# Kernel tuning notes

Hardware: AMD Instinct MI355X
Metric: run time of the kernel (lower is better)

## Reference

```python
import jax, jax.numpy as jnp
import numpy as np

GAMMA = 0.1
EPS = 1e-10


def setup_inputs() -> dict:
    key = jax.random.key(0)
    ks = jax.random.split(key, 7)
    B, N, D = 1024, 2048, 128
    return {
        "target_embed": jax.random.normal(ks[0], (B, D), dtype=jnp.float32),
        "candidate_embeds": jax.random.normal(ks[1], (B, N, D), dtype=jnp.float32),
        "Wq": jax.random.normal(ks[2], (D, D), dtype=jnp.float32) * 0.05,
        "bq": jax.random.normal(ks[3], (D,), dtype=jnp.float32) * 0.05,
        "Wk": jax.random.normal(ks[4], (D, D), dtype=jnp.float32) * 0.05,
        "bk": jax.random.normal(ks[5], (D,), dtype=jnp.float32) * 0.05,
        "u": jax.random.uniform(ks[6], (B, N), dtype=jnp.float32),
        "num_neighbors": 32,
    }


def reference(target_embed, candidate_embeds, Wq, bq, Wk, bk, u, num_neighbors):
    B, N, D = candidate_embeds.shape
    scale = jnp.sqrt(jnp.float32(D))
    # Linear projections (torch Linear: x @ W.T + b)
    Q = target_embed @ Wq.T + bq                      # [B, D]
    K = jnp.einsum('bnd,ed->bne', candidate_embeds, Wk) + bk  # [B, N, D]
    scores = jnp.einsum('bd,bnd->bn', Q, K) / scale   # [B, N]
    p = jax.nn.softmax(scores, axis=-1)
    p = (1.0 - GAMMA) * p + GAMMA / N                 # mix with uniform
    # multinomial without replacement == Gumbel top-k on log-probs
    gumbel = -jnp.log(-jnp.log(u + EPS) + EPS)        # [B, N]
    _, sampled_idx = jax.lax.top_k(jnp.log(p) + gumbel, num_neighbors)  # [B, k]
    return sampled_idx
```

## Files before the change

### kernel.cpp

```cpp
#include <hip/hip_runtime.h>
#include <cmath>
#include <cfloat>

constexpr int D  = 128;
constexpr int NT = 512;
constexpr int NW = NT / 64;
constexpr float EPS_ = 1e-10f;

__global__ __launch_bounds__(NT, 8) void adaptive_sampler_kernel(
    const float* __restrict__ target,
    const float* __restrict__ cand,
    const float* __restrict__ Wq,
    const float* __restrict__ bq,
    const float* __restrict__ Wk,
    const float* __restrict__ u,
    const int*   __restrict__ kptr,
    int*         __restrict__ out,
    int N)
{
  extern __shared__ float sS[];
  __shared__ float sTgt[D];
  __shared__ float sQ[D];
  __shared__ float sQt[D];
  __shared__ float redV[NW];
  __shared__ int   redI[NW];

  const int b    = blockIdx.x;
  const int tid  = threadIdx.x;
  const int lane = tid & 63;
  const int wave = tid >> 6;

  if (tid < D) sTgt[tid] = target[(size_t)b * D + tid];
  __syncthreads();

  if (tid < D) {
    float acc = 0.f;
    const float* wrow = Wq + (size_t)tid * D;
    #pragma unroll 8
    for (int e = 0; e < D; ++e) acc += sTgt[e] * wrow[e];
    sQ[tid] = acc + bq[tid];
  }
  __syncthreads();

  if (tid < D) {
    float acc = 0.f;
    #pragma unroll 8
    for (int d = 0; d < D; ++d) acc += sQ[d] * Wk[(size_t)d * D + tid];
    sQt[tid] = acc;
  }
  __syncthreads();

  const int grp = lane >> 4;
  const int gl  = lane & 15;
  float q0 = sQt[gl * 8 + 0], q1 = sQt[gl * 8 + 1];
  float q2 = sQt[gl * 8 + 2], q3 = sQt[gl * 8 + 3];
  float q4 = sQt[gl * 8 + 4], q5 = sQt[gl * 8 + 5];
  float q6 = sQt[gl * 8 + 6], q7 = sQt[gl * 8 + 7];

  const float scale = sqrtf((float)D);
  const int rstride = NW * 4;

  int n = wave * 4 + grp;
  for (; n + rstride < N; n += 2 * rstride) {
    const float4* r0 = (const float4*)(cand + ((size_t)b * N + n) * D);
    const float4* r1 = (const float4*)(cand + ((size_t)b * N + n + rstride) * D);
    float4 a0 = r0[gl * 2 + 0];
    float4 a1 = r0[gl * 2 + 1];
    float4 c0 = r1[gl * 2 + 0];
    float4 c1 = r1[gl * 2 + 1];
    float p0 = a0.x * q0 + a0.y * q1 + a0.z * q2 + a0.w * q3
             + a1.x * q4 + a1.y * q5 + a1.z * q6 + a1.w * q7;
    float p1 = c0.x * q0 + c0.y * q1 + c0.z * q2 + c0.w * q3
             + c1.x * q4 + c1.y * q5 + c1.z * q6 + c1.w * q7;
    p0 += __shfl_xor(p0, 1);  p1 += __shfl_xor(p1, 1);
    p0 += __shfl_xor(p0, 2);  p1 += __shfl_xor(p1, 2);
    p0 += __shfl_xor(p0, 4);  p1 += __shfl_xor(p1, 4);
    p0 += __shfl_xor(p0, 8);  p1 += __shfl_xor(p1, 8);
    if (gl == 0) { sS[n] = p0 / scale; sS[n + rstride] = p1 / scale; }
  }
  if (n < N) {
    const float4* r0 = (const float4*)(cand + ((size_t)b * N + n) * D);
    float4 a0 = r0[gl * 2 + 0];
    float4 a1 = r0[gl * 2 + 1];
    float p0 = a0.x * q0 + a0.y * q1 + a0.z * q2 + a0.w * q3
             + a1.x * q4 + a1.y * q5 + a1.z * q6 + a1.w * q7;
    p0 += __shfl_xor(p0, 1);
    p0 += __shfl_xor(p0, 2);
    p0 += __shfl_xor(p0, 4);
    p0 += __shfl_xor(p0, 8);
    if (gl == 0) sS[n] = p0 / scale;
  }
  __syncthreads();

  float m = -FLT_MAX;
  for (int i = tid; i < N; i += NT) m = fmaxf(m, sS[i]);
  for (int s = 32; s; s >>= 1) m = fmaxf(m, __shfl_xor(m, s));
  if (lane == 0) redV[wave] = m;
  __syncthreads();
  m = redV[0];
  #pragma unroll
  for (int w = 1; w < NW; ++w) m = fmaxf(m, redV[w]);
  __syncthreads();

  float ssum = 0.f;
  for (int i = tid; i < N; i += NT) ssum += expf(sS[i] - m);
  for (int s = 32; s; s >>= 1) ssum += __shfl_xor(ssum, s);
  if (lane == 0) redV[wave] = ssum;
  __syncthreads();
  float Z = redV[0];
  #pragma unroll
  for (int w = 1; w < NW; ++w) Z += redV[w];
  __syncthreads();

  const float mixc = (float)(0.1 / (double)N);
  for (int i = tid; i < N; i += NT) {
    float pmix = 0.9f * (expf(sS[i] - m) / Z) + mixc;
    float uv = u[(size_t)b * N + i];
    float g = -logf(-logf(uv + EPS_) + EPS_);
    sS[i] = logf(pmix) + g;
  }
  __syncthreads();

  const int k = kptr[0];
  for (int i = 0; i < k; ++i) {
    float bv = -FLT_MAX;
    int   bi = N;
    for (int j = tid; j < N; j += NT) {
      float v = sS[j];
      if (v > bv || (v == bv && j < bi)) { bv = v; bi = j; }
    }
    for (int s = 32; s; s >>= 1) {
      float ov = __shfl_xor(bv, s);
      int   oi = __shfl_xor(bi, s);
      if (ov > bv || (ov == bv && oi < bi)) { bv = ov; bi = oi; }
    }
    if (lane == 0) { redV[wave] = bv; redI[wave] = bi; }
    __syncthreads();
    if (tid == 0) {
      float fv = redV[0]; int fi = redI[0];
      #pragma unroll
      for (int w = 1; w < NW; ++w) {
        if (redV[w] > fv || (redV[w] == fv && redI[w] < fi)) {
          fv = redV[w]; fi = redI[w];
        }
      }
      out[(size_t)b * k + i] = fi;
      sS[fi] = -FLT_MAX;
    }
    __syncthreads();
  }
}

extern "C" void kernel_launch(void* const* d_in, const int* in_sizes, int n_in,
                              void* d_out, int out_size, void* d_ws, size_t ws_size,
                              hipStream_t stream) {
  const float* target = (const float*)d_in[0];
  const float* cand   = (const float*)d_in[1];
  const float* Wq     = (const float*)d_in[2];
  const float* bq     = (const float*)d_in[3];
  const float* Wk     = (const float*)d_in[4];
  const float* bk     = (const float*)d_in[5];
  const float* u      = (const float*)d_in[6];
  const int*   kptr   = (const int*)d_in[7];
  (void)bk;
  (void)n_in; (void)d_ws; (void)ws_size; (void)out_size;

  const int B = in_sizes[0] / D;
  const int N = in_sizes[1] / (B * D);

  adaptive_sampler_kernel<<<B, NT, N * sizeof(float), stream>>>(
      target, cand, Wq, bq, Wk, u, kptr, (int*)d_out, N);
}
```

Before: 256.6 us.

## Split sampler into projection, chunked score, and register-resident top-k kernels

Splits the fused kernel into three kernels when workspace allows. A projection kernel computes the query vector, a score kernel spreads each batch row's 2048 candidates over four blocks to raise parallelism on the bandwidth-bound dot products, and a top-k kernel keeps scores in registers, does a per-wave top-k and merges candidates in one wave. This replaces k block-wide barriers with wave-level work. The cost is extra launches and a workspace round-trip for the scores. It falls back to the fused kernel if workspace is too small, and the default path depends on ws_size.

```diff
diff --git a/kernel.cpp b/kernel.cpp
--- a/kernel.cpp
+++ b/kernel.cpp
@@ -1,38 +1,193 @@
 #include <hip/hip_runtime.h>
 #include <cmath>
 #include <cfloat>
-
-constexpr int D  = 128;
-constexpr int NT = 512;
-constexpr int NW = NT / 64;
+#include <climits>
+
+constexpr int D    = 128;
 constexpr float EPS_ = 1e-10f;
-
-__global__ __launch_bounds__(NT, 8) void adaptive_sampler_kernel(
-    const float* __restrict__ target,
-    const float* __restrict__ cand,
-    const float* __restrict__ Wq,
-    const float* __restrict__ bq,
-    const float* __restrict__ Wk,
-    const float* __restrict__ u,
-    const int*   __restrict__ kptr,
-    int*         __restrict__ out,
-    int N)
+constexpr int KMAX = 64;
+
+__global__ __launch_bounds__(128) void proj_kernel(
+    const float* __restrict__ target, const float* __restrict__ Wq,
+    const float* __restrict__ bq, const float* __restrict__ Wk,
+    float* __restrict__ qt)
+{
+  __shared__ float sTgt[D];
+  __shared__ float sQ[D];
+  const int b = blockIdx.x, tid = threadIdx.x;
+  sTgt[tid] = target[(size_t)b * D + tid];
+  __syncthreads();
+  float acc = 0.f;
+  const float* wrow = Wq + (size_t)tid * D;
+  #pragma unroll 8
+  for (int e = 0; e < D; ++e) acc += sTgt[e] * wrow[e];
+  sQ[tid] = acc + bq[tid];
+  __syncthreads();
+  acc = 0.f;
+  #pragma unroll 8
+  for (int d = 0; d < D; ++d) acc += sQ[d] * Wk[(size_t)d * D + tid];
+  qt[(size_t)b * D + tid] = acc;
+}
+
+constexpr int NT1 = 256;
+__global__ __launch_bounds__(NT1, 8) void score_kernel(
+    const float* __restrict__ cand, const float* __restrict__ qt,
+    float* __restrict__ scores, int N, int rows_per_blk)
+{
+  const int b    = blockIdx.x;
+  const int tid  = threadIdx.x;
+  const int lane = tid & 63;
+  const int wave = tid >> 6;
+  const int grp  = lane >> 4;
+  const int gl   = lane & 15;
+
+  const float* qp = qt + (size_t)b * D + gl * 8;
+  float4 qa = ((const float4*)qp)[0];
+  float4 qb = ((const float4*)qp)[1];
+
+  const float scale = sqrtf((float)D);
+  const int n0 = blockIdx.y * rows_per_blk;
+  const int n1 = n0 + rows_per_blk;
+  const float* base = cand + (size_t)b * N * D;
+  float* srow = scores + (size_t)b * N;
+
+  for (int n = n0 + wave * 4 + grp; n < n1; n += 32) {
+    const float4* r0 = (const float4*)(base + (size_t)n * D);
+    const float4* r1 = (const float4*)(base + (size_t)(n + 16) * D);
+    float4 a0 = r0[gl * 2 + 0];
+    float4 a1 = r0[gl * 2 + 1];
+    float4 c0 = r1[gl * 2 + 0];
+    float4 c1 = r1[gl * 2 + 1];
+    float p0 = a0.x * qa.x + a0.y * qa.y + a0.z * qa.z + a0.w * qa.w
+             + a1.x * qb.x + a1.y * qb.y + a1.z * qb.z + a1.w * qb.w;
+    float p1 = c0.x * qa.x + c0.y * qa.y + c0.z * qa.z + c0.w * qa.w
+             + c1.x * qb.x + c1.y * qb.y + c1.z * qb.z + c1.w * qb.w;
+    p0 += __shfl_xor(p0, 1);  p1 += __shfl_xor(p1, 1);
+    p0 += __shfl_xor(p0, 2);  p1 += __shfl_xor(p1, 2);
+    p0 += __shfl_xor(p0, 4);  p1 += __shfl_xor(p1, 4);
+    p0 += __shfl_xor(p0, 8);  p1 += __shfl_xor(p1, 8);
+    if (gl == 0) { srow[n] = p0 / scale; srow[n + 16] = p1 / scale; }
+  }
+}
+
+constexpr int NT2 = 256;
+__global__ __launch_bounds__(NT2) void topk_kernel(
+    const float* __restrict__ scores, const float* __restrict__ u,
+    const int* __restrict__ kptr, int* __restrict__ out, int N)
+{
+  __shared__ float redM[4];
+  __shared__ float redS[4];
+  __shared__ float cV[4 * KMAX];
+  __shared__ int   cI[4 * KMAX];
+
+  const int b    = blockIdx.x;
+  const int tid  = threadIdx.x;
+  const int lane = tid & 63;
+  const int wave = tid >> 6;
+  const int base = wave * 512 + lane * 8;
+
+  const float* srow = scores + (size_t)b * N;
+  float4 s0 = ((const float4*)(srow + base))[0];
+  float4 s1 = ((const float4*)(srow + base))[1];
+  float v[8] = { s0.x, s0.y, s0.z, s0.w, s1.x, s1.y, s1.z, s1.w };
+
+  float m = v[0];
+  #pragma unroll
+  for (int j = 1; j < 8; ++j) m = fmaxf(m, v[j]);
+  for (int s = 32; s; s >>= 1) m = fmaxf(m, __shfl_xor(m, s));
+  if (lane == 0) redM[wave] = m;
+  __syncthreads();
+  m = fmaxf(fmaxf(redM[0], redM[1]), fmaxf(redM[2], redM[3]));
+
+  float ssum = 0.f;
+  #pragma unroll
+  for (int j = 0; j < 8; ++j) ssum += expf(v[j] - m);
+  for (int s = 32; s; s >>= 1) ssum += __shfl_xor(ssum, s);
+  if (lane == 0) redS[wave] = ssum;
+  __syncthreads();
+  const float Z = redS[0] + redS[1] + redS[2] + redS[3];
+
+  const float mixc = (float)(0.1 / (double)N);
+  const float* urow = u + (size_t)b * N;
+  float4 u0 = ((const float4*)(urow + base))[0];
+  float4 u1 = ((const float4*)(urow + base))[1];
+  float uu[8] = { u0.x, u0.y, u0.z, u0.w, u1.x, u1.y, u1.z, u1.w };
+  #pragma unroll
+  for (int j = 0; j < 8; ++j) {
+    float pmix = 0.9f * (expf(v[j] - m) / Z) + mixc;
+    float g = -logf(-logf(uu[j] + EPS_) + EPS_);
+    v[j] = logf(pmix) + g;
+  }
+
+  const int k = kptr[0];
+
+  for (int i = 0; i < k; ++i) {
+    float bv = v[0]; int bj = 0;
+    #pragma unroll
+    for (int j = 1; j < 8; ++j) if (v[j] > bv) { bv = v[j]; bj = j; }
+    int bidx = base + bj;
+    for (int s = 32; s; s >>= 1) {
+      float ov = __shfl_xor(bv, s);
+      int   oi = __shfl_xor(bidx, s);
+      if (ov > bv || (ov == bv && oi < bidx)) { bv = ov; bidx = oi; }
+    }
+    if (lane == ((bidx - wave * 512) >> 3)) {
+      int off = bidx & 7;
+      #pragma unroll
+      for (int j = 0; j < 8; ++j) if (off == j) v[j] = -FLT_MAX;
+    }
+    if (lane == 0) { cV[wave * KMAX + i] = bv; cI[wave * KMAX + i] = bidx; }
+  }
+  __syncthreads();
+
+  if (wave == 0) {
+    const int tot = 4 * k;
+    float mv[4]; int mi[4];
+    #pragma unroll
+    for (int t = 0; t < 4; ++t) {
+      int c = lane + 64 * t;
+      if (c < tot) {
+        int w = c / k, i = c % k;
+        mv[t] = cV[w * KMAX + i]; mi[t] = cI[w * KMAX + i];
+      } else { mv[t] = -FLT_MAX; mi[t] = INT_MAX; }
+    }
+    for (int i = 0; i < k; ++i) {
+      float bv = mv[0]; int bidx = mi[0];
+      #pragma unroll
+      for (int t = 1; t < 4; ++t)
+        if (mv[t] > bv || (mv[t] == bv && mi[t] < bidx)) { bv = mv[t]; bidx = mi[t]; }
+      for (int s = 32; s; s >>= 1) {
+        float ov = __shfl_xor(bv, s);
+        int   oi = __shfl_xor(bidx, s);
+        if (ov > bv || (ov == bv && oi < bidx)) { bv = ov; bidx = oi; }
+      }
+      #pragma unroll
+      for (int t = 0; t < 4; ++t) if (mi[t] == bidx) mv[t] = -FLT_MAX;
+      if (lane == 0) out[(size_t)b * k + i] = bidx;
+    }
+  }
+}
+
+constexpr int NTF = 512;
+constexpr int NWF = NTF / 64;
+__global__ __launch_bounds__(NTF, 8) void fused_kernel(
+    const float* __restrict__ target, const float* __restrict__ cand,
+    const float* __restrict__ Wq, const float* __restrict__ bq,
+    const float* __restrict__ Wk, const float* __restrict__ u,
+    const int* __restrict__ kptr, int* __restrict__ out, int N)
 {
   extern __shared__ float sS[];
   __shared__ float sTgt[D];
   __shared__ float sQ[D];
   __shared__ float sQt[D];
-  __shared__ float redV[NW];
-  __shared__ int   redI[NW];
-
-  const int b    = blockIdx.x;
-  const int tid  = threadIdx.x;
-  const int lane = tid & 63;
-  const int wave = tid >> 6;
+  __shared__ float redV[NWF];
+  __shared__ int   redI[NWF];
+
+  const int b = blockIdx.x, tid = threadIdx.x;
+  const int lane = tid & 63, wave = tid >> 6;
 
   if (tid < D) sTgt[tid] = target[(size_t)b * D + tid];
   __syncthreads();
-
   if (tid < D) {
     float acc = 0.f;
     const float* wrow = Wq + (size_t)tid * D;
@@ -41,7 +196,6 @@
     sQ[tid] = acc + bq[tid];
   }
   __syncthreads();
-
   if (tid < D) {
     float acc = 0.f;
     #pragma unroll 8
@@ -50,70 +204,55 @@
   }
   __syncthreads();
 
-  const int grp = lane >> 4;
-  const int gl  = lane & 15;
-  float q0 = sQt[gl * 8 + 0], q1 = sQt[gl * 8 + 1];
-  float q2 = sQt[gl * 8 + 2], q3 = sQt[gl * 8 + 3];
-  float q4 = sQt[gl * 8 + 4], q5 = sQt[gl * 8 + 5];
-  float q6 = sQt[gl * 8 + 6], q7 = sQt[gl * 8 + 7];
-
+  const int grp = lane >> 4, gl = lane & 15;
+  float q0 = sQt[gl*8+0], q1 = sQt[gl*8+1], q2 = sQt[gl*8+2], q3 = sQt[gl*8+3];
+  float q4 = sQt[gl*8+4], q5 = sQt[gl*8+5], q6 = sQt[gl*8+6], q7 = sQt[gl*8+7];
   const float scale = sqrtf((float)D);
-  const int rstride = NW * 4;
-
+  const int rstride = NWF * 4;
   int n = wave * 4 + grp;
   for (; n + rstride < N; n += 2 * rstride) {
     const float4* r0 = (const float4*)(cand + ((size_t)b * N + n) * D);
     const float4* r1 = (const float4*)(cand + ((size_t)b * N + n + rstride) * D);
-    float4 a0 = r0[gl * 2 + 0];
-    float4 a1 = r0[gl * 2 + 1];
-    float4 c0 = r1[gl * 2 + 0];
-    float4 c1 = r1[gl * 2 + 1];
-    float p0 = a0.x * q0 + a0.y * q1 + a0.z * q2 + a0.w * q3
-             + a1.x * q4 + a1.y * q5 + a1.z * q6 + a1.w * q7;
-    float p1 = c0.x * q0 + c0.y * q1 + c0.z * q2 + c0.w * q3
-             + c1.x * q4 + c1.y * q5 + c1.z * q6 + c1.w * q7;
-    p0 += __shfl_xor(p0, 1);  p1 += __shfl_xor(p1, 1);
-    p0 += __shfl_xor(p0, 2);  p1 += __shfl_xor(p1, 2);
-    p0 += __shfl_xor(p0, 4);  p1 += __shfl_xor(p1, 4);
-    p0 += __shfl_xor(p0, 8);  p1 += __shfl_xor(p1, 8);
+    float4 a0 = r0[gl*2+0], a1 = r0[gl*2+1], c0 = r1[gl*2+0], c1 = r1[gl*2+1];
+    float p0 = a0.x*q0 + a0.y*q1 + a0.z*q2 + a0.w*q3 + a1.x*q4 + a1.y*q5 + a1.z*q6 + a1.w*q7;
+    float p1 = c0.x*q0 + c0.y*q1 + c0.z*q2 + c0.w*q3 + c1.x*q4 + c1.y*q5 + c1.z*q6 + c1.w*q7;
+    p0 += __shfl_xor(p0,1); p1 += __shfl_xor(p1,1);
+    p0 += __shfl_xor(p0,2); p1 += __shfl_xor(p1,2);
+    p0 += __shfl_xor(p0,4); p1 += __shfl_xor(p1,4);
+    p0 += __shfl_xor(p0,8); p1 += __shfl_xor(p1,8);
     if (gl == 0) { sS[n] = p0 / scale; sS[n + rstride] = p1 / scale; }
   }
   if (n < N) {
     const float4* r0 = (const float4*)(cand + ((size_t)b * N + n) * D);
-    float4 a0 = r0[gl * 2 + 0];
-    float4 a1 = r0[gl * 2 + 1];
-    float p0 = a0.x * q0 + a0.y * q1 + a0.z * q2 + a0.w * q3
-             + a1.x * q4 + a1.y * q5 + a1.z * q6 + a1.w * q7;
-    p0 += __shfl_xor(p0, 1);
-    p0 += __shfl_xor(p0, 2);
-    p0 += __shfl_xor(p0, 4);
-    p0 += __shfl_xor(p0, 8);
+    float4 a0 = r0[gl*2+0], a1 = r0[gl*2+1];
+    float p0 = a0.x*q0 + a0.y*q1 + a0.z*q2 + a0.w*q3 + a1.x*q4 + a1.y*q5 + a1.z*q6 + a1.w*q7;
+    p0 += __shfl_xor(p0,1); p0 += __shfl_xor(p0,2); p0 += __shfl_xor(p0,4); p0 += __shfl_xor(p0,8);
     if (gl == 0) sS[n] = p0 / scale;
   }
   __syncthreads();
 
   float m = -FLT_MAX;
-  for (int i = tid; i < N; i += NT) m = fmaxf(m, sS[i]);
+  for (int i = tid; i < N; i += NTF) m = fmaxf(m, sS[i]);
   for (int s = 32; s; s >>= 1) m = fmaxf(m, __shfl_xor(m, s));
   if (lane == 0) redV[wave] = m;
   __syncthreads();
   m = redV[0];
   #pragma unroll
-  for (int w = 1; w < NW; ++w) m = fmaxf(m, redV[w]);
+  for (int w = 1; w < NWF; ++w) m = fmaxf(m, redV[w]);
   __syncthreads();
 
   float ssum = 0.f;
-  for (int i = tid; i < N; i += NT) ssum += expf(sS[i] - m);
+  for (int i = tid; i < N; i += NTF) ssum += expf(sS[i] - m);
   for (int s = 32; s; s >>= 1) ssum += __shfl_xor(ssum, s);
   if (lane == 0) redV[wave] = ssum;
   __syncthreads();
   float Z = redV[0];
   #pragma unroll
-  for (int w = 1; w < NW; ++w) Z += redV[w];
+  for (int w = 1; w < NWF; ++w) Z += redV[w];
   __syncthreads();
 
   const float mixc = (float)(0.1 / (double)N);
-  for (int i = tid; i < N; i += NT) {
+  for (int i = tid; i < N; i += NTF) {
     float pmix = 0.9f * (expf(sS[i] - m) / Z) + mixc;
     float uv = u[(size_t)b * N + i];
     float g = -logf(-logf(uv + EPS_) + EPS_);
@@ -123,15 +262,13 @@
 
   const int k = kptr[0];
   for (int i = 0; i < k; ++i) {
-    float bv = -FLT_MAX;
-    int   bi = N;
-    for (int j = tid; j < N; j += NT) {
-      float v = sS[j];
-      if (v > bv || (v == bv && j < bi)) { bv = v; bi = j; }
+    float bv = -FLT_MAX; int bi = N;
+    for (int j = tid; j < N; j += NTF) {
+      float vv = sS[j];
+      if (vv > bv || (vv == bv && j < bi)) { bv = vv; bi = j; }
     }
     for (int s = 32; s; s >>= 1) {
-      float ov = __shfl_xor(bv, s);
-      int   oi = __shfl_xor(bi, s);
+      float ov = __shfl_xor(bv, s); int oi = __shfl_xor(bi, s);
       if (ov > bv || (ov == bv && oi < bi)) { bv = ov; bi = oi; }
     }
     if (lane == 0) { redV[wave] = bv; redI[wave] = bi; }
@@ -139,11 +276,8 @@
     if (tid == 0) {
       float fv = redV[0]; int fi = redI[0];
       #pragma unroll
-      for (int w = 1; w < NW; ++w) {
-        if (redV[w] > fv || (redV[w] == fv && redI[w] < fi)) {
-          fv = redV[w]; fi = redI[w];
-        }
-      }
+      for (int w = 1; w < NWF; ++w)
+        if (redV[w] > fv || (redV[w] == fv && redI[w] < fi)) { fv = redV[w]; fi = redI[w]; }
       out[(size_t)b * k + i] = fi;
       sS[fi] = -FLT_MAX;
     }
@@ -162,12 +296,26 @@
   const float* bk     = (const float*)d_in[5];
   const float* u      = (const float*)d_in[6];
   const int*   kptr   = (const int*)d_in[7];
-  (void)bk;
-  (void)n_in; (void)d_ws; (void)ws_size; (void)out_size;
+  (void)bk; (void)n_in;
 
   const int B = in_sizes[0] / D;
   const int N = in_sizes[1] / (B * D);
-
-  adaptive_sampler_kernel<<<B, NT, N * sizeof(float), stream>>>(
-      target, cand, Wq, bq, Wk, u, kptr, (int*)d_out, N);
-}
+  const int k = out_size / B;
+
+  const size_t need = ((size_t)B * N + (size_t)B * D) * sizeof(float);
+  const bool ok3 = (ws_size >= need) && (N == NT2 * 8) && (k <= KMAX) &&
+                   (N % 128 == 0);
+
+  if (ok3) {
+    float* scores = (float*)d_ws;
+    float* qt     = scores + (size_t)B * N;
+    proj_kernel<<<B, 128, 0, stream>>>(target, Wq, bq, Wk, qt);
+    const int chunks = 4;
+    const int rows_per_blk = N / chunks;
+    score_kernel<<<dim3(B, chunks), NT1, 0, stream>>>(cand, qt, scores, N, rows_per_blk);
+    topk_kernel<<<B, NT2, 0, stream>>>(scores, u, kptr, (int*)d_out, N);
+  } else {
+    fused_kernel<<<B, NTF, N * sizeof(float), stream>>>(
+        target, cand, Wq, bq, Wk, u, kptr, (int*)d_out, N);
+  }
+}
```

Measured after the change: 271.1 us. 5.6% more time.
